# Kernel tuning notes

Hardware: AMD Instinct MI355X
Metric: run time of the kernel (lower is better)

## Reference

```python
import jax, jax.numpy as jnp
import numpy as np

NH, NKV, HD = 32, 8, 64      # query heads, kv heads, head dim
H, INTER = 2048, 8192        # hidden, mlp intermediate
B, NBLK, BS = 32, 256, 16    # batch, blocks per seq, block size
NUM_BLOCKS = B * NBLK
EPS = 1e-5
THETA = 10000.0


def rms_norm(x, w):
    var = jnp.mean(x * x, axis=-1, keepdims=True)
    return x * jax.lax.rsqrt(var + EPS) * w


def rotate_half(x):
    x1, x2 = jnp.split(x, 2, axis=-1)
    return jnp.concatenate([-x2, x1], axis=-1)


def setup_inputs() -> dict:
    key = jax.random.key(0)
    ks = jax.random.split(key, 12)
    s = 0.02
    x = jax.random.normal(ks[0], (B, 1, H), jnp.float32)
    k_cache = jax.random.normal(ks[1], (NUM_BLOCKS, BS, NKV, HD), jnp.float32)
    v_cache = jax.random.normal(ks[2], (NUM_BLOCKS, BS, NKV, HD), jnp.float32)
    block_table = jnp.arange(B * NBLK, dtype=jnp.int32).reshape(B, NBLK)
    cache_seqlens = jax.random.randint(ks[3], (B,), 0, NBLK * BS - 1, jnp.int32)
    return {
        'x': x, 'k_cache': k_cache, 'v_cache': v_cache,
        'ln1_w': jnp.ones((H,), jnp.float32),
        'q_w': jax.random.normal(ks[4], (H, NH * HD), jnp.float32) * s,
        'k_w': jax.random.normal(ks[5], (H, NKV * HD), jnp.float32) * s,
        'v_w': jax.random.normal(ks[6], (H, NKV * HD), jnp.float32) * s,
        'o_w': jax.random.normal(ks[7], (NH * HD, H), jnp.float32) * s,
        'ln2_w': jnp.ones((H,), jnp.float32),
        'gate_w': jax.random.normal(ks[8], (H, INTER), jnp.float32) * s,
        'up_w': jax.random.normal(ks[9], (H, INTER), jnp.float32) * s,
        'down_w': jax.random.normal(ks[10], (INTER, H), jnp.float32) * s,
        'block_table': block_table,
        'cache_seqlens': cache_seqlens,
        'block_size': BS,
    }


def reference(x, k_cache, v_cache, ln1_w, q_w, k_w, v_w, o_w, ln2_w,
              gate_w, up_w, down_w, block_table, cache_seqlens, block_size):
    b = x.shape[0]
    normed = rms_norm(x, ln1_w)[:, 0, :]                     # [B,H]
    q = (normed @ q_w).reshape(b, NH, HD)                    # [B,NH,HD]
    k = (normed @ k_w).reshape(b, NKV, HD)                   # [B,NKV,HD]
    v = (normed @ v_w).reshape(b, NKV, HD)

    # RoPE at current position (HF rotate_half convention)
    pos = cache_seqlens.astype(jnp.float32)                  # [B]
    inv_freq = 1.0 / (THETA ** (jnp.arange(0, HD, 2, dtype=jnp.float32) / HD))
    ang = pos[:, None] * inv_freq[None, :]                   # [B,HD/2]
    cos = jnp.concatenate([jnp.cos(ang), jnp.cos(ang)], -1)[:, None, :]  # [B,1,HD]
    sin = jnp.concatenate([jnp.sin(ang), jnp.sin(ang)], -1)[:, None, :]
    q = q * cos + rotate_half(q) * sin
    k = k * cos + rotate_half(k) * sin

    # paged cache update: write new k/v at block_table[b, pos//bs], offset pos%bs
    blk = block_table[jnp.arange(b), cache_seqlens // block_size]
    flat_idx = blk.astype(jnp.int32) * block_size + cache_seqlens % block_size  # [B]
    kc = k_cache.reshape(-1, NKV, HD).at[flat_idx].set(k).reshape(k_cache.shape)
    vc = v_cache.reshape(-1, NKV, HD).at[flat_idx].set(v).reshape(v_cache.shape)

    # gather paged KV via block table -> [B, S, NKV, HD]
    K = kc[block_table].reshape(b, -1, NKV, HD)
    V = vc[block_table].reshape(b, -1, NKV, HD)
    S = K.shape[1]

    # decode attention with GQA: head h uses kv head h // (NH//NKV)
    G = NH // NKV
    qh = q.reshape(b, NKV, G, HD)
    scores = jnp.einsum('bkgd,bskd->bkgs', qh, K) / jnp.sqrt(jnp.float32(HD))
    valid = (jnp.arange(S)[None, :] <= cache_seqlens[:, None])  # seqlen+1 tokens
    scores = jnp.where(valid[:, None, None, :], scores, -jnp.inf)
    probs = jax.nn.softmax(scores, axis=-1)
    attn = jnp.einsum('bkgs,bskd->bkgd', probs, V).reshape(b, NH * HD)

    x = x + (attn @ o_w)[:, None, :]

    h = rms_norm(x, ln2_w)
    mlp = (jax.nn.silu(h @ gate_w) * (h @ up_w)) @ down_w
    return x + mlp
```

## Files before the change

kernel.cpp:

```cpp
#include <hip/hip_runtime.h>
#include <math.h>

#define B_      32
#define H_      2048
#define NH_     32
#define NKV_    8
#define HD_     64
#define G_      4
#define INTER_  8192
#define NBLK_   256
#define BS_     16
#define NCHUNK_ 8
#define CHUNK_  512

#define OFF_NORMED_T 0
#define OFF_QKV_P    65536
#define OFF_QROPE    1638400
#define OFF_HT       1703936
#define OFF_ATTN_T   1769472
#define OFF_GU_P     1835008
#define OFF_ACT_T    6029312
#define OFF_O_P      6291456
#define OFF_D_P      7340032
#define OFF_OPART    9437184
#define OFF_MPART    9961472
#define OFF_LPART    9969664

__global__ __launch_bounds__(256) void rmsnorm_kernel(const float* __restrict__ xin,
                                                      const float* __restrict__ w,
                                                      float* __restrict__ out_t) {
    int b = blockIdx.x, tid = threadIdx.x;
    const float* xr = xin + (size_t)b * H_;
    float xv[8];
    float ss = 0.f;
#pragma unroll
    for (int j = 0; j < 8; ++j) {
        xv[j] = xr[tid + j * 256];
        ss += xv[j] * xv[j];
    }
#pragma unroll
    for (int off = 32; off >= 1; off >>= 1) ss += __shfl_xor(ss, off, 64);
    __shared__ float red[4];
    __shared__ float rbc;
    if ((tid & 63) == 0) red[tid >> 6] = ss;
    __syncthreads();
    if (tid == 0) rbc = rsqrtf((red[0] + red[1] + red[2] + red[3]) / (float)H_ + 1e-5f);
    __syncthreads();
    float r = rbc;
#pragma unroll
    for (int j = 0; j < 8; ++j) {
        int i = tid + j * 256;
        out_t[(size_t)i * B_ + b] = xv[j] * r * w[i];
    }
}

__device__ __forceinline__ void gemv4_block(const float* __restrict__ xt,
                                            const float* __restrict__ W, int Nw,
                                            int wcol0, int rowsPerWave,
                                            float* __restrict__ part, int Nout,
                                            int outcol0) {
    int tid = threadIdx.x;
    int lane = tid & 63;
    int ks = tid >> 6;
    int k0 = (blockIdx.y * 4 + ks) * rowsPerWave;
    int wcol = wcol0 + lane * 4;

    float acc[4][B_];
#pragma unroll
    for (int c = 0; c < 4; ++c)
#pragma unroll
        for (int b = 0; b < B_; ++b) acc[c][b] = 0.f;

    const float* Wp = W + (size_t)k0 * Nw + wcol;
    const float* xp = xt + (size_t)k0 * B_;
#pragma unroll 2
    for (int k = 0; k < rowsPerWave; ++k) {
        float4 w4 = *(const float4*)(Wp + (size_t)k * Nw);
        const float* xr = xp + k * B_;
#pragma unroll
        for (int b = 0; b < B_; ++b) {
            float xv = xr[b];
            acc[0][b] = fmaf(w4.x, xv, acc[0][b]);
            acc[1][b] = fmaf(w4.y, xv, acc[1][b]);
            acc[2][b] = fmaf(w4.z, xv, acc[2][b]);
            acc[3][b] = fmaf(w4.w, xv, acc[3][b]);
        }
    }

    __shared__ float red[4][2][260];
    float* prow = part + (size_t)blockIdx.y * B_ * Nout;
    for (int b0 = 0; b0 < B_; b0 += 2) {
#pragma unroll
        for (int bi = 0; bi < 2; ++bi)
#pragma unroll
            for (int c = 0; c < 4; ++c)
                red[ks][bi][lane * 4 + c] = acc[c][b0 + bi];
        __syncthreads();
#pragma unroll
        for (int bi = 0; bi < 2; ++bi) {
            float s = red[0][bi][tid] + red[1][bi][tid] + red[2][bi][tid] + red[3][bi][tid];
            prow[(size_t)(b0 + bi) * Nout + outcol0 + tid] = s;
        }
        __syncthreads();
    }
}

__global__ __launch_bounds__(256, 2) void gemv_qkv_kernel(const float* __restrict__ xt,
                                                          const float* __restrict__ qw,
                                                          const float* __restrict__ kw,
                                                          const float* __restrict__ vw,
                                                          float* __restrict__ part) {
    int cb = blockIdx.x;
    if (cb < 8)       gemv4_block(xt, qw, 2048, cb * 256, 32, part, 3072, cb * 256);
    else if (cb < 10) gemv4_block(xt, kw, 512, (cb - 8) * 256, 32, part, 3072, cb * 256);
    else              gemv4_block(xt, vw, 512, (cb - 10) * 256, 32, part, 3072, cb * 256);
}

__global__ __launch_bounds__(256, 2) void gemv_o_kernel(const float* __restrict__ xt,
                                                        const float* __restrict__ W,
                                                        float* __restrict__ part) {
    gemv4_block(xt, W, 2048, blockIdx.x * 256, 32, part, 2048, blockIdx.x * 256);
}

__global__ __launch_bounds__(256, 2) void gemv_gateup_kernel(const float* __restrict__ xt,
                                                             const float* __restrict__ gw,
                                                             const float* __restrict__ uw,
                                                             float* __restrict__ part) {
    int cb = blockIdx.x;
    if (cb < 32) gemv4_block(xt, gw, 8192, cb * 256, 64, part, 16384, cb * 256);
    else         gemv4_block(xt, uw, 8192, (cb - 32) * 256, 64, part, 16384, 8192 + (cb - 32) * 256);
}

__global__ __launch_bounds__(256, 2) void gemv_down_kernel(const float* __restrict__ xt,
                                                           const float* __restrict__ W,
                                                           float* __restrict__ part) {
    gemv4_block(xt, W, 2048, blockIdx.x * 256, 64, part, 2048, blockIdx.x * 256);
}

__global__ __launch_bounds__(256) void qkv_reduce_rope_kernel(const float* __restrict__ part,
                                                              const int* __restrict__ btab,
                                                              const int* __restrict__ seql,
                                                              float* __restrict__ qrope,
                                                              float* __restrict__ kc,
                                                              float* __restrict__ vc) {
    int b = blockIdx.x, tid = threadIdx.x;
    __shared__ float s[3072];
#pragma unroll
    for (int j = 0; j < 12; ++j) {
        int col = tid + j * 256;
        float a = 0.f;
#pragma unroll
        for (int y = 0; y < 16; ++y) a += part[((size_t)y * B_ + b) * 3072 + col];
        s[col] = a;
    }
    __syncthreads();
    int pos = seql[b];
    float fpos = (float)pos;
    const float LOG2T = 13.287712379549449f;
#pragma unroll
    for (int j = 0; j < 8; ++j) {
        int i = tid + j * 256;
        int d = i & 63, ii = d & 31;
        float ang = fpos * exp2f(-(float)(2 * ii) * (LOG2T / 64.f));
        float c = cosf(ang), sn = sinf(ang);
        float v1 = s[i], v2 = s[(d < 32) ? i + 32 : i - 32];
        qrope[(size_t)b * 2048 + i] = (d < 32) ? (v1 * c - v2 * sn) : (v1 * c + v2 * sn);
    }
    int blk = btab[b * NBLK_ + (pos >> 4)];
    size_t cbase = (size_t)(blk * BS_ + (pos & 15)) * NKV_ * HD_;
    for (int i = tid; i < NKV_ * HD_; i += 256) {
        int d = i & 63, ii = d & 31;
        float ang = fpos * exp2f(-(float)(2 * ii) * (LOG2T / 64.f));
        float c = cosf(ang), sn = sinf(ang);
        float v1 = s[2048 + i], v2 = s[2048 + ((d < 32) ? i + 32 : i - 32)];
        kc[cbase + i] = (d < 32) ? (v1 * c - v2 * sn) : (v1 * c + v2 * sn);
        vc[cbase + i] = s[2560 + i];
    }
}

__global__ __launch_bounds__(256, 4) void attn_chunk_kernel(const float* __restrict__ qrope,
                                                            const float* __restrict__ kc,
                                                            const float* __restrict__ vc,
                                                            const int* __restrict__ btab,
                                                            const int* __restrict__ seqlens,
                                                            float* __restrict__ opart,
                                                            float* __restrict__ mpart,
                                                            float* __restrict__ lpart) {
    int cx = blockIdx.x, kv = blockIdx.y, b = blockIdx.z;
    int tid = threadIdx.x;
    int pos = seqlens[b];
    int c0 = cx * CHUNK_;
    int pidx = ((b * NKV_ + kv) * NCHUNK_ + cx) * G_;
    if (c0 > pos) {
        if (tid < G_) { mpart[pidx + tid] = -__builtin_inff(); lpart[pidx + tid] = 0.f; }
        return;
    }
    __shared__ float qlds[G_][HD_];
    __shared__ float slds[G_][CHUNK_];
    __shared__ float vt[32][HD_];
    __shared__ int btl[32];
    if (tid < 32) btl[tid] = btab[b * NBLK_ + (c0 >> 4) + tid];
    {
        int h = tid >> 6, d = tid & 63;
        qlds[h][d] = qrope[((size_t)b * NH_ + kv * G_ + h) * HD_ + d] * 0.125f;
    }
    __syncthreads();

    int grp = tid >> 4, ln = tid & 15;
    for (int tb = 0; tb < CHUNK_; tb += 16) {
        int tl = tb + grp;
        int t = c0 + tl;
        int blk = btl[tl >> 4];
        const float4 k4 = *(const float4*)(kc + ((size_t)(blk * BS_ + (t & 15)) * NKV_ + kv) * HD_ + ln * 4);
        bool valid = (t <= pos);
#pragma unroll
        for (int h = 0; h < G_; ++h) {
            const float4 q4 = *(const float4*)&qlds[h][ln * 4];
            float p = q4.x * k4.x + q4.y * k4.y + q4.z * k4.z + q4.w * k4.w;
#pragma unroll
            for (int off = 8; off >= 1; off >>= 1) p += __shfl_xor(p, off, 16);
            if (ln == 0) slds[h][tl] = valid ? p : -__builtin_inff();
        }
    }
    __syncthreads();

    int h = tid >> 6, lane = tid & 63;
    float m = -__builtin_inff();
    for (int i = lane; i < CHUNK_; i += 64) m = fmaxf(m, slds[h][i]);
#pragma unroll
    for (int off = 32; off >= 1; off >>= 1) m = fmaxf(m, __shfl_xor(m, off, 64));
    float l = 0.f;
    for (int i = lane; i < CHUNK_; i += 64) {
        float p = expf(slds[h][i] - m);
        slds[h][i] = p;
        l += p;
    }
#pragma unroll
    for (int off = 32; off >= 1; off >>= 1) l += __shfl_xor(l, off, 64);
    if (lane == 0) { mpart[pidx + h] = m; lpart[pidx + h] = l; }
    __syncthreads();

    int d = lane;
    float o = 0.f;
    int tmax = min(CHUNK_, pos + 1 - c0);
    for (int t0 = 0; t0 < tmax; t0 += 32) {
#pragma unroll
        for (int r = 0; r < 2; ++r) {
            int tl = t0 + r * 16 + (tid >> 4);
            int t = c0 + tl;
            int blk = btl[tl >> 4];
            *(float4*)&vt[r * 16 + (tid >> 4)][(tid & 15) * 4] =
                *(const float4*)(vc + ((size_t)(blk * BS_ + (t & 15)) * NKV_ + kv) * HD_ + (tid & 15) * 4);
        }
        __syncthreads();
#pragma unroll 8
        for (int tl2 = 0; tl2 < 32; ++tl2)
            o = fmaf(slds[h][t0 + tl2], vt[tl2][d], o);
        __syncthreads();
    }
    opart[(size_t)(pidx + h) * HD_ + d] = o;
}

__global__ __launch_bounds__(64) void attn_reduce_kernel(const float* __restrict__ opart,
                                                         const float* __restrict__ mpart,
                                                         const float* __restrict__ lpart,
                                                         float* __restrict__ attn_t) {
    int hq = blockIdx.x, b = blockIdx.y;
    int kv = hq >> 2, g = hq & 3;
    int lane = threadIdx.x;
    int base = ((b * NKV_ + kv) * NCHUNK_) * G_ + g;
    float mv[NCHUNK_], lv[NCHUNK_];
    float M = -__builtin_inff();
#pragma unroll
    for (int c = 0; c < NCHUNK_; ++c) {
        mv[c] = mpart[base + c * G_];
        lv[c] = lpart[base + c * G_];
        M = fmaxf(M, mv[c]);
    }
    float L = 0.f, o = 0.f;
#pragma unroll
    for (int c = 0; c < NCHUNK_; ++c) {
        if (lv[c] > 0.f) {
            float f = expf(mv[c] - M);
            L += lv[c] * f;
            o += f * opart[(size_t)(base + c * G_) * HD_ + lane];
        }
    }
    attn_t[(size_t)(hq * HD_ + lane) * B_ + b] = o / L;
}

__global__ __launch_bounds__(256) void o_reduce_rms2_kernel(const float* __restrict__ part,
                                                            const float* __restrict__ x,
                                                            const float* __restrict__ w2,
                                                            float* __restrict__ out,
                                                            float* __restrict__ ht) {
    int b = blockIdx.x, tid = threadIdx.x;
    float v[8];
    float ss = 0.f;
#pragma unroll
    for (int j = 0; j < 8; ++j) {
        int col = tid + j * 256;
        float a = x[(size_t)b * H_ + col];
#pragma unroll
        for (int y = 0; y < 16; ++y) a += part[((size_t)y * B_ + b) * 2048 + col];
        v[j] = a;
        ss += a * a;
    }
#pragma unroll
    for (int off = 32; off >= 1; off >>= 1) ss += __shfl_xor(ss, off, 64);
    __shared__ float red[4];
    __shared__ float rbc;
    if ((tid & 63) == 0) red[tid >> 6] = ss;
    __syncthreads();
    if (tid == 0) rbc = rsqrtf((red[0] + red[1] + red[2] + red[3]) / (float)H_ + 1e-5f);
    __syncthreads();
    float r = rbc;
#pragma unroll
    for (int j = 0; j < 8; ++j) {
        int col = tid + j * 256;
        out[(size_t)b * H_ + col] = v[j];
        ht[(size_t)col * B_ + b] = v[j] * r * w2[col];
    }
}

__global__ __launch_bounds__(256) void gu_reduce_silu_kernel(const float* __restrict__ part,
                                                             float* __restrict__ act_t) {
    int j0 = blockIdx.x * 64, tid = threadIdx.x;
    int jj = tid & 63, bq = tid >> 6;
    __shared__ float tile[64][33];
#pragma unroll
    for (int bb = 0; bb < 8; ++bb) {
        int b = bq * 8 + bb;
        float g = 0.f, u = 0.f;
#pragma unroll
        for (int y = 0; y < 8; ++y) {
            size_t base = ((size_t)y * B_ + b) * 16384 + j0 + jj;
            g += part[base];
            u += part[base + 8192];
        }
        tile[jj][b] = (g / (1.f + expf(-g))) * u;
    }
    __syncthreads();
#pragma unroll
    for (int r = 0; r < 8; ++r) {
        int j = r * 8 + (tid >> 5);
        int bc = tid & 31;
        act_t[(size_t)(j0 + j) * B_ + bc] = tile[j][bc];
    }
}

__global__ __launch_bounds__(256) void down_reduce_kernel(const float* __restrict__ part,
                                                          float* __restrict__ out) {
    int idx = blockIdx.x * 256 + threadIdx.x;
    float a = out[idx];
#pragma unroll
    for (int y = 0; y < 32; ++y) a += part[(size_t)y * 65536 + idx];
    out[idx] = a;
}

extern "C" void kernel_launch(void* const* d_in, const int* in_sizes, int n_in,
                              void* d_out, int out_size, void* d_ws, size_t ws_size,
                              hipStream_t stream) {
    const float* x       = (const float*)d_in[0];
    float*       k_cache = (float*)d_in[1];
    float*       v_cache = (float*)d_in[2];
    const float* ln1_w   = (const float*)d_in[3];
    const float* q_w     = (const float*)d_in[4];
    const float* k_w     = (const float*)d_in[5];
    const float* v_w     = (const float*)d_in[6];
    const float* o_w     = (const float*)d_in[7];
    const float* ln2_w   = (const float*)d_in[8];
    const float* gate_w  = (const float*)d_in[9];
    const float* up_w    = (const float*)d_in[10];
    const float* down_w  = (const float*)d_in[11];
    const int*   btab    = (const int*)d_in[12];
    const int*   seql    = (const int*)d_in[13];
    float* out = (float*)d_out;

    float* ws = (float*)d_ws;
    float* normed_t = ws + OFF_NORMED_T;
    float* qkv_p    = ws + OFF_QKV_P;
    float* qrope    = ws + OFF_QROPE;
    float* ht       = ws + OFF_HT;
    float* attn_t   = ws + OFF_ATTN_T;
    float* gu_p     = ws + OFF_GU_P;
    float* act_t    = ws + OFF_ACT_T;
    float* o_p      = ws + OFF_O_P;
    float* d_p      = ws + OFF_D_P;
    float* opart    = ws + OFF_OPART;
    float* mpart    = ws + OFF_MPART;
    float* lpart    = ws + OFF_LPART;

    rmsnorm_kernel<<<32, 256, 0, stream>>>(x, ln1_w, normed_t);
    gemv_qkv_kernel<<<dim3(12, 16), 256, 0, stream>>>(normed_t, q_w, k_w, v_w, qkv_p);
    qkv_reduce_rope_kernel<<<32, 256, 0, stream>>>(qkv_p, btab, seql, qrope, k_cache, v_cache);
    attn_chunk_kernel<<<dim3(NCHUNK_, NKV_, B_), 256, 0, stream>>>(qrope, k_cache, v_cache,
                                                                   btab, seql, opart, mpart, lpart);
    attn_reduce_kernel<<<dim3(NH_, B_), 64, 0, stream>>>(opart, mpart, lpart, attn_t);
    gemv_o_kernel<<<dim3(8, 16), 256, 0, stream>>>(attn_t, o_w, o_p);
    o_reduce_rms2_kernel<<<32, 256, 0, stream>>>(o_p, x, ln2_w, out, ht);
    gemv_gateup_kernel<<<dim3(64, 8), 256, 0, stream>>>(ht, gate_w, up_w, gu_p);
    gu_reduce_silu_kernel<<<128, 256, 0, stream>>>(gu_p, act_t);
    gemv_down_kernel<<<dim3(8, 32), 256, 0, stream>>>(act_t, down_w, d_p);
    down_reduce_kernel<<<256, 256, 0, stream>>>(d_p, out);
}
```

Measured before the change: 779.9 us.

## Restructure attention chunk kernel to per-thread tokens and split O-proj GEMV further

The attention chunk kernel now gives each thread a whole token for QK dot products across all four grouped heads, which removes the 16-lane shuffle reductions. For PV, each wave takes its own slice of tokens and reads V directly instead of staging it through shared memory with per-tile barriers, then combines wave results in LDS. The O-projection GEMV doubles its K-split to 32 slices for more blocks, which also grows the partial-sum buffer, shifts workspace offsets and adds work to the reduce. Per-thread K row reads are strided across lanes and less coalesced, which is a risk to memory efficiency.

```diff
diff --git a/kernel.cpp b/kernel.cpp
--- a/kernel.cpp
+++ b/kernel.cpp
@@ -21,10 +21,10 @@
 #define OFF_GU_P     1835008
 #define OFF_ACT_T    6029312
 #define OFF_O_P      6291456
-#define OFF_D_P      7340032
-#define OFF_OPART    9437184
-#define OFF_MPART    9961472
-#define OFF_LPART    9969664
+#define OFF_D_P      8388608
+#define OFF_OPART    10485760
+#define OFF_MPART    11010048
+#define OFF_LPART    11018240
 
 __global__ __launch_bounds__(256) void rmsnorm_kernel(const float* __restrict__ xin,
                                                       const float* __restrict__ w,
@@ -61,7 +61,7 @@
                                             int outcol0) {
     int tid = threadIdx.x;
     int lane = tid & 63;
-    int ks = tid >> 6;
+    int ks = __builtin_amdgcn_readfirstlane(tid >> 6);
     int k0 = (blockIdx.y * 4 + ks) * rowsPerWave;
     int wcol = wcol0 + lane * 4;
 
@@ -119,7 +119,7 @@
 __global__ __launch_bounds__(256, 2) void gemv_o_kernel(const float* __restrict__ xt,
                                                         const float* __restrict__ W,
                                                         float* __restrict__ part) {
-    gemv4_block(xt, W, 2048, blockIdx.x * 256, 32, part, 2048, blockIdx.x * 256);
+    gemv4_block(xt, W, 2048, blockIdx.x * 256, 16, part, 2048, blockIdx.x * 256);
 }
 
 __global__ __launch_bounds__(256, 2) void gemv_gateup_kernel(const float* __restrict__ xt,
@@ -191,13 +191,14 @@
     int pos = seqlens[b];
     int c0 = cx * CHUNK_;
     int pidx = ((b * NKV_ + kv) * NCHUNK_ + cx) * G_;
+    float ninf = -__builtin_inff();
     if (c0 > pos) {
-        if (tid < G_) { mpart[pidx + tid] = -__builtin_inff(); lpart[pidx + tid] = 0.f; }
+        if (tid < G_) { mpart[pidx + tid] = ninf; lpart[pidx + tid] = 0.f; }
         return;
     }
     __shared__ float qlds[G_][HD_];
     __shared__ float slds[G_][CHUNK_];
-    __shared__ float vt[32][HD_];
+    __shared__ float ored[4][G_][HD_];
     __shared__ int btl[32];
     if (tid < 32) btl[tid] = btab[b * NBLK_ + (c0 >> 4) + tid];
     {
@@ -206,59 +207,94 @@
     }
     __syncthreads();
 
-    int grp = tid >> 4, ln = tid & 15;
-    for (int tb = 0; tb < CHUNK_; tb += 16) {
-        int tl = tb + grp;
+    int w = tid >> 6, lane = tid & 63;
+
+    for (int sub = 0; sub < 2; ++sub) {
+        int tl = w * 128 + sub * 64 + lane;
         int t = c0 + tl;
         int blk = btl[tl >> 4];
-        const float4 k4 = *(const float4*)(kc + ((size_t)(blk * BS_ + (t & 15)) * NKV_ + kv) * HD_ + ln * 4);
+        const float* kp = kc + ((size_t)(blk * BS_ + (t & 15)) * NKV_ + kv) * HD_;
+        float p0 = 0.f, p1 = 0.f, p2 = 0.f, p3 = 0.f;
+#pragma unroll 8
+        for (int i = 0; i < 16; ++i) {
+            float4 k4 = *(const float4*)(kp + i * 4);
+            float4 q0 = *(const float4*)&qlds[0][i * 4];
+            float4 q1 = *(const float4*)&qlds[1][i * 4];
+            float4 q2 = *(const float4*)&qlds[2][i * 4];
+            float4 q3 = *(const float4*)&qlds[3][i * 4];
+            p0 += q0.x * k4.x + q0.y * k4.y + q0.z * k4.z + q0.w * k4.w;
+            p1 += q1.x * k4.x + q1.y * k4.y + q1.z * k4.z + q1.w * k4.w;
+            p2 += q2.x * k4.x + q2.y * k4.y + q2.z * k4.z + q2.w * k4.w;
+            p3 += q3.x * k4.x + q3.y * k4.y + q3.z * k4.z + q3.w * k4.w;
+        }
         bool valid = (t <= pos);
-#pragma unroll
-        for (int h = 0; h < G_; ++h) {
-            const float4 q4 = *(const float4*)&qlds[h][ln * 4];
-            float p = q4.x * k4.x + q4.y * k4.y + q4.z * k4.z + q4.w * k4.w;
-#pragma unroll
-            for (int off = 8; off >= 1; off >>= 1) p += __shfl_xor(p, off, 16);
-            if (ln == 0) slds[h][tl] = valid ? p : -__builtin_inff();
-        }
-    }
-    __syncthreads();
-
-    int h = tid >> 6, lane = tid & 63;
-    float m = -__builtin_inff();
-    for (int i = lane; i < CHUNK_; i += 64) m = fmaxf(m, slds[h][i]);
-#pragma unroll
-    for (int off = 32; off >= 1; off >>= 1) m = fmaxf(m, __shfl_xor(m, off, 64));
-    float l = 0.f;
-    for (int i = lane; i < CHUNK_; i += 64) {
-        float p = expf(slds[h][i] - m);
-        slds[h][i] = p;
-        l += p;
-    }
-#pragma unroll
-    for (int off = 32; off >= 1; off >>= 1) l += __shfl_xor(l, off, 64);
-    if (lane == 0) { mpart[pidx + h] = m; lpart[pidx + h] = l; }
-    __syncthreads();
-
-    int d = lane;
-    float o = 0.f;
+        slds[0][tl] = valid ? p0 : ninf;
+        slds[1][tl] = valid ? p1 : ninf;
+        slds[2][tl] = valid ? p2 : ninf;
+        slds[3][tl] = valid ? p3 : ninf;
+    }
+    __syncthreads();
+
+    {
+        int h = w;
+        float m = ninf;
+        for (int i = lane; i < CHUNK_; i += 64) m = fmaxf(m, slds[h][i]);
+#pragma unroll
+        for (int off = 32; off >= 1; off >>= 1) m = fmaxf(m, __shfl_xor(m, off, 64));
+        float l = 0.f;
+        for (int i = lane; i < CHUNK_; i += 64) {
+            float p = expf(slds[h][i] - m);
+            slds[h][i] = p;
+            l += p;
+        }
+#pragma unroll
+        for (int off = 32; off >= 1; off >>= 1) l += __shfl_xor(l, off, 64);
+        if (lane == 0) { mpart[pidx + h] = m; lpart[pidx + h] = l; }
+    }
+    __syncthreads();
+
+    int g = lane >> 4, cq = lane & 15;
+    float4 o0 = {0,0,0,0}, o1 = {0,0,0,0}, o2 = {0,0,0,0}, o3 = {0,0,0,0};
     int tmax = min(CHUNK_, pos + 1 - c0);
-    for (int t0 = 0; t0 < tmax; t0 += 32) {
-#pragma unroll
-        for (int r = 0; r < 2; ++r) {
-            int tl = t0 + r * 16 + (tid >> 4);
-            int t = c0 + tl;
-            int blk = btl[tl >> 4];
-            *(float4*)&vt[r * 16 + (tid >> 4)][(tid & 15) * 4] =
-                *(const float4*)(vc + ((size_t)(blk * BS_ + (t & 15)) * NKV_ + kv) * HD_ + (tid & 15) * 4);
-        }
-        __syncthreads();
-#pragma unroll 8
-        for (int tl2 = 0; tl2 < 32; ++tl2)
-            o = fmaf(slds[h][t0 + tl2], vt[tl2][d], o);
-        __syncthreads();
-    }
-    opart[(size_t)(pidx + h) * HD_ + d] = o;
+    int start = w * 128;
+    int end = min(start + 128, tmax);
+    for (int t0 = start; t0 < end; t0 += 4) {
+        int tl = t0 + g;
+        int t = c0 + tl;
+        int blk = btl[tl >> 4];
+        const float4 v4 = *(const float4*)(vc + ((size_t)(blk * BS_ + (t & 15)) * NKV_ + kv) * HD_ + cq * 4);
+        float pv0 = slds[0][tl], pv1 = slds[1][tl], pv2 = slds[2][tl], pv3 = slds[3][tl];
+        o0.x = fmaf(pv0, v4.x, o0.x); o0.y = fmaf(pv0, v4.y, o0.y);
+        o0.z = fmaf(pv0, v4.z, o0.z); o0.w = fmaf(pv0, v4.w, o0.w);
+        o1.x = fmaf(pv1, v4.x, o1.x); o1.y = fmaf(pv1, v4.y, o1.y);
+        o1.z = fmaf(pv1, v4.z, o1.z); o1.w = fmaf(pv1, v4.w, o1.w);
+        o2.x = fmaf(pv2, v4.x, o2.x); o2.y = fmaf(pv2, v4.y, o2.y);
+        o2.z = fmaf(pv2, v4.z, o2.z); o2.w = fmaf(pv2, v4.w, o2.w);
+        o3.x = fmaf(pv3, v4.x, o3.x); o3.y = fmaf(pv3, v4.y, o3.y);
+        o3.z = fmaf(pv3, v4.z, o3.z); o3.w = fmaf(pv3, v4.w, o3.w);
+    }
+#pragma unroll
+    for (int mask = 16; mask <= 32; mask <<= 1) {
+        o0.x += __shfl_xor(o0.x, mask, 64); o0.y += __shfl_xor(o0.y, mask, 64);
+        o0.z += __shfl_xor(o0.z, mask, 64); o0.w += __shfl_xor(o0.w, mask, 64);
+        o1.x += __shfl_xor(o1.x, mask, 64); o1.y += __shfl_xor(o1.y, mask, 64);
+        o1.z += __shfl_xor(o1.z, mask, 64); o1.w += __shfl_xor(o1.w, mask, 64);
+        o2.x += __shfl_xor(o2.x, mask, 64); o2.y += __shfl_xor(o2.y, mask, 64);
+        o2.z += __shfl_xor(o2.z, mask, 64); o2.w += __shfl_xor(o2.w, mask, 64);
+        o3.x += __shfl_xor(o3.x, mask, 64); o3.y += __shfl_xor(o3.y, mask, 64);
+        o3.z += __shfl_xor(o3.z, mask, 64); o3.w += __shfl_xor(o3.w, mask, 64);
+    }
+    if (g == 0) {
+        *(float4*)&ored[w][0][cq * 4] = o0;
+        *(float4*)&ored[w][1][cq * 4] = o1;
+        *(float4*)&ored[w][2][cq * 4] = o2;
+        *(float4*)&ored[w][3][cq * 4] = o3;
+    }
+    __syncthreads();
+    {
+        float s = ored[0][w][lane] + ored[1][w][lane] + ored[2][w][lane] + ored[3][w][lane];
+        opart[(size_t)(pidx + w) * HD_ + lane] = s;
+    }
 }
 
 __global__ __launch_bounds__(64) void attn_reduce_kernel(const float* __restrict__ opart,
@@ -302,7 +338,7 @@
         int col = tid + j * 256;
         float a = x[(size_t)b * H_ + col];
 #pragma unroll
-        for (int y = 0; y < 16; ++y) a += part[((size_t)y * B_ + b) * 2048 + col];
+        for (int y = 0; y < 32; ++y) a += part[((size_t)y * B_ + b) * 2048 + col];
         v[j] = a;
         ss += a * a;
     }
@@ -397,7 +433,7 @@
     attn_chunk_kernel<<<dim3(NCHUNK_, NKV_, B_), 256, 0, stream>>>(qrope, k_cache, v_cache,
                                                                    btab, seql, opart, mpart, lpart);
     attn_reduce_kernel<<<dim3(NH_, B_), 64, 0, stream>>>(opart, mpart, lpart, attn_t);
-    gemv_o_kernel<<<dim3(8, 16), 256, 0, stream>>>(attn_t, o_w, o_p);
+    gemv_o_kernel<<<dim3(8, 32), 256, 0, stream>>>(attn_t, o_w, o_p);
     o_reduce_rms2_kernel<<<32, 256, 0, stream>>>(o_p, x, ln2_w, out, ht);
     gemv_gateup_kernel<<<dim3(64, 8), 256, 0, stream>>>(ht, gate_w, up_w, gu_p);
     gu_reduce_silu_kernel<<<128, 256, 0, stream>>>(gu_p, act_t);
```

Measured after the change: 810.0 us. 1.04x slower.
